# Kernel optimization log

Measured on AMD Instinct MI355X. Metric: run time of the kernel, lower is better.

The kernel has to match this reference:

```python
import jax, jax.numpy as jnp
import numpy as np

BN_EPS = 1e-5

def batchnorm(x, gamma, beta):
    # training-mode BatchNorm1d over the row (node/sample) dimension
    mu = jnp.mean(x, axis=0)
    var = jnp.var(x, axis=0)
    return (x - mu) * jax.lax.rsqrt(var + BN_EPS) * gamma + beta

def gin_mean(h, src, dst, n):
    # DGL GINConv(apply_func=None, aggregator='mean', eps=0):
    # h_new = h + mean_{u in N(v)} h_u
    ones = jnp.ones((src.shape[0],), h.dtype)
    deg = jax.ops.segment_sum(ones, dst, num_segments=n)
    agg = jax.ops.segment_sum(h[src], dst, num_segments=n)
    return h + agg / jnp.maximum(deg, 1.0)[:, None]

def setup_inputs() -> dict:
    key = jax.random.key(0)
    ks = jax.random.split(key, 12)
    N, E, B, K = 10000, 160000, 64, 10
    DIN, D, DH = 20, 512, 256
    x = jax.random.normal(ks[0], (N, DIN), dtype=jnp.float32)
    edge_src = jax.random.randint(ks[1], (E,), 0, N, dtype=jnp.int32)
    edge_dst = jax.random.randint(ks[2], (E,), 0, N, dtype=jnp.int32)
    node2graph = jnp.sort(jax.random.randint(ks[3], (N,), 0, B, dtype=jnp.int32))
    pg_emb = jax.random.normal(ks[4], (B, D), dtype=jnp.float32)
    neigh_emb = jax.random.normal(ks[5], (B, K, D), dtype=jnp.float32)
    s = lambda i, shp: jax.random.normal(ks[i], shp, dtype=jnp.float32) * 0.02
    return dict(
        x=x, pg_emb=pg_emb, neigh_emb=neigh_emb,
        W_init=s(6, (DIN, D)), b_init=jnp.zeros((D,), jnp.float32),
        g1=jnp.ones((D,), jnp.float32), be1=jnp.zeros((D,), jnp.float32),
        g2=jnp.ones((D,), jnp.float32), be2=jnp.zeros((D,), jnp.float32),
        W_fc=s(7, (3 * D, DH)), b_fc=jnp.zeros((DH,), jnp.float32),
        W_fc2=s(8, (DH, DH)), b_fc2=jnp.zeros((DH,), jnp.float32),
        W_fc3=s(9, (DH, DH)), b_fc3=jnp.zeros((DH,), jnp.float32),
        W_fc4=s(10, (DH, 1)), b_fc4=jnp.zeros((1,), jnp.float32),
        gb=jnp.ones((DH,), jnp.float32), bb=jnp.zeros((DH,), jnp.float32),
        gb2=jnp.ones((DH,), jnp.float32), bb2=jnp.zeros((DH,), jnp.float32),
        gb3=jnp.ones((DH,), jnp.float32), bb3=jnp.zeros((DH,), jnp.float32),
        edge_src=edge_src, edge_dst=edge_dst, node2graph=node2graph,
    )

def reference(x, pg_emb, neigh_emb, W_init, b_init, g1, be1, g2, be2,
              W_fc, b_fc, W_fc2, b_fc2, W_fc3, b_fc3, W_fc4, b_fc4,
              gb, bb, gb2, bb2, gb3, bb3, edge_src, edge_dst, node2graph):
    N = x.shape[0]
    B, K, D = neigh_emb.shape
    # two GIN(mean) layers with BN+ReLU on the batched graph
    h = x @ W_init + b_init                                   # [N, 512]
    h = jax.nn.relu(batchnorm(gin_mean(h, edge_src, edge_dst, N), g1, be1))
    h = jax.nn.relu(batchnorm(gin_mean(h, edge_src, edge_dst, N), g2, be2))
    # dgl.mean_nodes: per-graph mean readout
    cnt = jax.ops.segment_sum(jnp.ones((N,), h.dtype), node2graph, num_segments=B)
    qemb = jax.ops.segment_sum(h, node2graph, num_segments=B) / jnp.maximum(cnt, 1.0)[:, None]
    a = jnp.concatenate([qemb, pg_emb], axis=1)               # [B, 2D]
    a = jnp.broadcast_to(a[:, None, :], (B, K, 2 * D))        # repeat per candidate
    b = jnp.concatenate([a, neigh_emb], axis=-1).reshape(B * K, 3 * D)
    H = jax.nn.relu(batchnorm(b @ W_fc + b_fc, gb, bb))
    H2 = jax.nn.relu(batchnorm(H @ W_fc2 + b_fc2, gb2, bb2))
    H3 = jax.nn.relu(batchnorm(H2 @ W_fc3 + b_fc3, gb3, bb3))
    pred = jax.nn.sigmoid(H3 @ W_fc4 + b_fc4)                 # [B*K, 1]
    return pred.reshape(B, K)
```

## Files before the change

### kernel.cpp

```cpp
#include <hip/hip_runtime.h>
#include <hip/hip_bf16.h>
#include <math.h>

#define N_NODES 10000
#define N_EDGES 160000
#define D 512
#define DIN 20
#define B 64
#define KC 10
#define DH 256
#define NROW (B*KC)
#define BN_EPS 1e-5f

#define ZCOUNT 36352
#define Z4 (ZCOUNT/4)
#define D4 (N_NODES/4)
#define IM_ROWS 8
#define IM_UNITS (N_NODES/IM_ROWS)
#define DEG_BLOCKS 625
#define GWAVES 4
#define GBLOCKS 1250
#define F1_NS 6
#define F1_ROWS 8
#define F1_KS 256
#define FM_ROWS 4
#define FM_KS 128
#define FM_NS 2

struct P {
  const float *x, *pg, *neigh, *Winit, *binit;
  const float *g1, *be1, *g2, *be2;
  const float *Wfc, *bfc, *W2, *b2, *W3, *b3, *W4, *b4;
  const float *gbA, *bbA, *gbB, *bbB, *gbC, *bbC;
  const int *esrc, *edst, *n2g;
  unsigned short *hb0, *hb1, *hb2;
  float *zbuf, *csum1, *csq1, *csum2, *csq2;
  float *s1,*q1,*s2,*q2,*s3,*q3, *qemb;
  float *G1,*G2,*G3,*part;
  int *degi,*rowstart,*cursor,*csr,*gstart;
  float *out;
};

__device__ __forceinline__ void f4acc(float4& a, const float4 v){
  a.x += v.x; a.y += v.y; a.z += v.z; a.w += v.w;
}
__device__ __forceinline__ void mk_affine(const float4 s, const float4 q, const float4 g,
                                          const float4 b, float4& sc, float4& sh){
  const float invN = 1.0f/(float)N_NODES;
  float mu, var, rs;
  mu = s.x*invN; var = q.x*invN - mu*mu; rs = rsqrtf(var+BN_EPS); sc.x = rs*g.x; sh.x = b.x - mu*sc.x;
  mu = s.y*invN; var = q.y*invN - mu*mu; rs = rsqrtf(var+BN_EPS); sc.y = rs*g.y; sh.y = b.y - mu*sc.y;
  mu = s.z*invN; var = q.z*invN - mu*mu; rs = rsqrtf(var+BN_EPS); sc.z = rs*g.z; sh.z = b.z - mu*sc.z;
  mu = s.w*invN; var = q.w*invN - mu*mu; rs = rsqrtf(var+BN_EPS); sc.w = rs*g.w; sh.w = b.w - mu*sc.w;
}
__device__ __forceinline__ float4 aff_relu(const float4 v, const float4 sc, const float4 sh){
  float4 o;
  o.x = fmaxf(fmaf(v.x, sc.x, sh.x), 0.0f);
  o.y = fmaxf(fmaf(v.y, sc.y, sh.y), 0.0f);
  o.z = fmaxf(fmaf(v.z, sc.z, sh.z), 0.0f);
  o.w = fmaxf(fmaf(v.w, sc.w, sh.w), 0.0f);
  return o;
}
__device__ __forceinline__ void bf_unpack(const uint4 u, float4& lo, float4& hi){
  lo.x = __uint_as_float(u.x << 16); lo.y = __uint_as_float(u.x & 0xffff0000u);
  lo.z = __uint_as_float(u.y << 16); lo.w = __uint_as_float(u.y & 0xffff0000u);
  hi.x = __uint_as_float(u.z << 16); hi.y = __uint_as_float(u.z & 0xffff0000u);
  hi.z = __uint_as_float(u.w << 16); hi.w = __uint_as_float(u.w & 0xffff0000u);
}
__device__ __forceinline__ unsigned bf_pack2(float a, float b){
  unsigned ua = __float_as_uint(a); ua = (ua + 0x7fffu + ((ua>>16)&1u)) >> 16;
  unsigned ub = __float_as_uint(b); ub = (ub + 0x7fffu + ((ub>>16)&1u)) & 0xffff0000u;
  return (ua & 0xffffu) | ub;
}
__device__ __forceinline__ unsigned short bf_pack1(float a){
  unsigned ua = __float_as_uint(a); return (unsigned short)((ua + 0x7fffu + ((ua>>16)&1u)) >> 16);
}

template<bool FUSED>
__device__ __forceinline__ void gather_body(const P& p,
    const unsigned short* __restrict__ hin, unsigned short* __restrict__ hout,
    const float* pcs, const float* pcq, const float* pgm, const float* pbt,
    float* cs, float* cq, float* red){
  int t = threadIdx.x;
  int lane = t & 63;
  int wave = t >> 6;
  int wid  = blockIdx.x*GWAVES + wave;
  int tot  = gridDim.x*GWAVES;
  const uint4* hb4 = (const uint4*)hin;
  float4 scA, shA, scB, shB;
  if (FUSED){
    mk_affine(((const float4*)pcs)[2*lane],   ((const float4*)pcq)[2*lane],
              ((const float4*)pgm)[2*lane],   ((const float4*)pbt)[2*lane],   scA, shA);
    mk_affine(((const float4*)pcs)[2*lane+1], ((const float4*)pcq)[2*lane+1],
              ((const float4*)pgm)[2*lane+1], ((const float4*)pbt)[2*lane+1], scB, shB);
  }
  float4 sLo = make_float4(0,0,0,0), sHi = make_float4(0,0,0,0);
  float4 qLo = make_float4(0,0,0,0), qHi = make_float4(0,0,0,0);
  for (int node = wid; node < N_NODES; node += tot){
    int start = p.rowstart[node], end = p.rowstart[node+1];
    float4 aLo = make_float4(0,0,0,0), aHi = make_float4(0,0,0,0);
    float4 bLo = make_float4(0,0,0,0), bHi = make_float4(0,0,0,0);
    for (int base = start; base < end; base += 64){
      int cnt = end - base; if (cnt > 64) cnt = 64;
      int myidx = (lane < cnt) ? p.csr[base+lane] : 0;
      int j = 0;
      for (; j+8 <= cnt; j += 8){
        uint4 u[8];
        #pragma unroll
        for (int k = 0; k < 8; ++k){
          int idx = __shfl(myidx, j+k, 64);
          u[k] = hb4[(size_t)idx*64 + lane];
        }
        #pragma unroll
        for (int k = 0; k < 8; ++k){
          float4 lo, hi; bf_unpack(u[k], lo, hi);
          if (FUSED){ lo = aff_relu(lo, scA, shA); hi = aff_relu(hi, scB, shB); }
          if (k & 1){ f4acc(bLo, lo); f4acc(bHi, hi); }
          else      { f4acc(aLo, lo); f4acc(aHi, hi); }
        }
      }
      for (; j < cnt; ++j){
        int idx = __shfl(myidx, j, 64);
        uint4 u0 = hb4[(size_t)idx*64 + lane];
        float4 lo, hi; bf_unpack(u0, lo, hi);
        if (FUSED){ lo = aff_relu(lo, scA, shA); hi = aff_relu(hi, scB, shB); }
        f4acc(aLo, lo); f4acc(aHi, hi);
      }
    }
    float inv = 1.0f/fmaxf((float)(end-start), 1.0f);
    uint4 us = hb4[(size_t)node*64 + lane];
    float4 hLo, hHi; bf_unpack(us, hLo, hHi);
    if (FUSED){ hLo = aff_relu(hLo, scA, shA); hHi = aff_relu(hHi, scB, shB); }
    float4 oLo, oHi;
    oLo.x = hLo.x + (aLo.x+bLo.x)*inv;  oLo.y = hLo.y + (aLo.y+bLo.y)*inv;
    oLo.z = hLo.z + (aLo.z+bLo.z)*inv;  oLo.w = hLo.w + (aLo.w+bLo.w)*inv;
    oHi.x = hHi.x + (aHi.x+bHi.x)*inv;  oHi.y = hHi.y + (aHi.y+bHi.y)*inv;
    oHi.z = hHi.z + (aHi.z+bHi.z)*inv;  oHi.w = hHi.w + (aHi.w+bHi.w)*inv;
    uint4 ou;
    ou.x = bf_pack2(oLo.x, oLo.y); ou.y = bf_pack2(oLo.z, oLo.w);
    ou.z = bf_pack2(oHi.x, oHi.y); ou.w = bf_pack2(oHi.z, oHi.w);
    ((uint4*)hout)[(size_t)node*64 + lane] = ou;
    f4acc(sLo, oLo); f4acc(sHi, oHi);
    qLo.x += oLo.x*oLo.x; qLo.y += oLo.y*oLo.y; qLo.z += oLo.z*oLo.z; qLo.w += oLo.w*oLo.w;
    qHi.x += oHi.x*oHi.x; qHi.y += oHi.y*oHi.y; qHi.z += oHi.z*oHi.z; qHi.w += oHi.w*oHi.w;
  }
  float* my = red + wave*1024;
  int c = 8*lane;
  *((float4*)&my[c])      = sLo;  *((float4*)&my[c+4])     = sHi;
  *((float4*)&my[512+c])  = qLo;  *((float4*)&my[512+c+4]) = qHi;
  __syncthreads();
  for (int e = t; e < 1024; e += 256){
    float v = red[e] + red[1024+e] + red[2048+e] + red[3072+e];
    if (e < 512) atomicAdd(&cs[e], v);
    else         atomicAdd(&cq[e-512], v);
  }
}

__global__ __launch_bounds__(256) void k_setup(P p){
  int b = blockIdx.x, nb = gridDim.x, t = threadIdx.x;
  for (int i4 = b*256 + t; i4 < Z4 + D4; i4 += nb*256){
    if (i4 < Z4) ((float4*)p.zbuf)[i4] = make_float4(0.f,0.f,0.f,0.f);
    else         ((int4*)p.degi)[i4 - Z4] = make_int4(0,0,0,0);
  }
  if (b == 0 && t <= B){
    int lo = 0, hi = N_NODES;
    while (lo < hi){ int mid = (lo+hi)>>1; if (p.n2g[mid] < t) lo = mid+1; else hi = mid; }
    p.gstart[t] = lo;
  }
}

__global__ __launch_bounds__(256) void k_deg_init(P p){
  __shared__ float xs[IM_ROWS*DIN];
  int t = threadIdx.x;
  if (blockIdx.x < DEG_BLOCKS){
    int e = blockIdx.x*256 + t;
    if (e < N_EDGES) atomicAdd(&p.degi[p.edst[e]], 1);
    return;
  }
  int unit = blockIdx.x - DEG_BLOCKS;
  float wlo[DIN], whi[DIN];
  #pragma unroll
  for (int k = 0; k < DIN; ++k){ wlo[k] = p.Winit[k*D + t]; whi[k] = p.Winit[k*D + t + 256]; }
  float b0 = p.binit[t], b1 = p.binit[t+256];
  int r0 = unit*IM_ROWS;
  for (int i = t; i < IM_ROWS*DIN; i += 256) xs[i] = p.x[(size_t)r0*DIN + i];
  __syncthreads();
  for (int rr = 0; rr < IM_ROWS; ++rr){
    float a0 = b0, a1 = b1;
    #pragma unroll
    for (int k = 0; k < DIN; ++k){
      float xv = xs[rr*DIN + k];
      a0 += xv*wlo[k]; a1 += xv*whi[k];
    }
    p.hb0[(size_t)(r0+rr)*D + t]       = bf_pack1(a0);
    p.hb0[(size_t)(r0+rr)*D + t + 256] = bf_pack1(a1);
  }
}

__global__ __launch_bounds__(256) void k_scan(P p){
  __shared__ int part[256];
  int t = threadIdx.x;
  const int PER = (N_NODES + 255)/256;
  int base = t*PER;
  int s = 0;
  for (int i = 0; i < PER; ++i){ int idx = base+i; if (idx < N_NODES) s += p.degi[idx]; }
  part[t] = s;
  __syncthreads();
  for (int off = 1; off < 256; off <<= 1){
    int v = (t >= off) ? part[t-off] : 0;
    __syncthreads();
    part[t] += v;
    __syncthreads();
  }
  int run = (t > 0) ? part[t-1] : 0;
  for (int i = 0; i < PER; ++i){
    int idx = base+i;
    if (idx < N_NODES){ p.rowstart[idx] = run; p.cursor[idx] = run; run += p.degi[idx]; }
  }
  if (t == 255) p.rowstart[N_NODES] = run;
}

__global__ __launch_bounds__(256) void k_fill(P p){
  int e = blockIdx.x*256 + threadIdx.x;
  if (e < N_EDGES){
    int pos = atomicAdd(&p.cursor[p.edst[e]], 1);
    p.csr[pos] = p.esrc[e];
  }
}

__global__ __launch_bounds__(256) void k_g1(P p){
  __shared__ float red[4096];
  gather_body<false>(p, p.hb0, p.hb1, nullptr,nullptr,nullptr,nullptr, p.csum1, p.csq1, red);
}
__global__ __launch_bounds__(256) void k_g2(P p){
  __shared__ float red[4096];
  gather_body<true>(p, p.hb1, p.hb2, p.csum1, p.csq1, p.g1, p.be1, p.csum2, p.csq2, red);
}

__global__ __launch_bounds__(256) void k_readout(P p){
  __shared__ float red[2048];
  int g = blockIdx.x >> 3, chunk = blockIdx.x & 7;
  int t = threadIdx.x;
  int lane = t & 63, wave = t >> 6;
  const uint4* hb4 = (const uint4*)p.hb2;
  float4 scA, shA, scB, shB;
  mk_affine(((const float4*)p.csum2)[2*lane],   ((const float4*)p.csq2)[2*lane],
            ((const float4*)p.g2)[2*lane],      ((const float4*)p.be2)[2*lane],   scA, shA);
  mk_affine(((const float4*)p.csum2)[2*lane+1], ((const float4*)p.csq2)[2*lane+1],
            ((const float4*)p.g2)[2*lane+1],    ((const float4*)p.be2)[2*lane+1], scB, shB);
  int s = p.gstart[g], e = p.gstart[g+1];
  int rows = e - s;
  int per = (rows + 7)/8;
  int r0 = s + chunk*per;
  int r1 = r0 + per; if (r1 > e) r1 = e;
  float4 aLo = make_float4(0,0,0,0), aHi = make_float4(0,0,0,0);
  for (int r = r0 + wave; r < r1; r += 4){
    uint4 u = hb4[(size_t)r*64 + lane];
    float4 lo, hi; bf_unpack(u, lo, hi);
    lo = aff_relu(lo, scA, shA); hi = aff_relu(hi, scB, shB);
    f4acc(aLo, lo); f4acc(aHi, hi);
  }
  int c = 8*lane;
  *((float4*)&red[wave*512 + c])     = aLo;
  *((float4*)&red[wave*512 + c + 4]) = aHi;
  __syncthreads();
  for (int e2 = t; e2 < 512; e2 += 256){
    float v = red[e2] + red[512+e2] + red[1024+e2] + red[1536+e2];
    atomicAdd(&p.qemb[(size_t)g*D + e2], v);
  }
}

__global__ __launch_bounds__(256) void k_fc1(P p){
  __shared__ float brow[F1_ROWS*F1_KS];
  int t = threadIdx.x;
  int rb = blockIdx.x % 80, ks = blockIdx.x / 80;
  int r0 = rb*F1_ROWS, k0 = ks*F1_KS;
  for (int rr = 0; rr < F1_ROWS; ++rr){
    int r = r0+rr;
    int g = r/KC, k = r - g*KC;
    int j = k0 + t;
    float v;
    if (j < D){
      float invc = 1.0f/fmaxf((float)(p.gstart[g+1]-p.gstart[g]), 1.0f);
      v = p.qemb[(size_t)g*D + j]*invc;
    } else if (j < 2*D){
      v = p.pg[(size_t)g*D + (j-D)];
    } else {
      v = p.neigh[((size_t)g*KC + k)*D + (j-2*D)];
    }
    brow[rr*F1_KS + t] = v;
  }
  __syncthreads();
  float acc[F1_ROWS] = {0.f,0.f,0.f,0.f,0.f,0.f,0.f,0.f};
  #pragma unroll 4
  for (int kk = 0; kk < F1_KS; ++kk){
    float w = p.Wfc[(size_t)(k0+kk)*DH + t];
    #pragma unroll
    for (int rr = 0; rr < F1_ROWS; ++rr) acc[rr] += brow[rr*F1_KS + kk]*w;
  }
  for (int rr = 0; rr < F1_ROWS; ++rr)
    p.part[((size_t)ks*NROW + r0+rr)*DH + t] = acc[rr];
}

__global__ __launch_bounds__(256) void k_reduce(P p, const float* bias, float* outG,
                                                float* s, float* q, int nslice){
  int t = threadIdx.x;
  int r0 = blockIdx.x*8;
  float bval = bias[t];
  float ls = 0.f, lq = 0.f;
  for (int rr = 0; rr < 8; ++rr){
    int r = r0+rr;
    float acc = bval;
    for (int sl = 0; sl < nslice; ++sl) acc += p.part[((size_t)sl*NROW + r)*DH + t];
    outG[(size_t)r*DH + t] = acc;
    ls += acc; lq += acc*acc;
  }
  atomicAdd(&s[t], ls); atomicAdd(&q[t], lq);
}

__global__ __launch_bounds__(256) void k_fcmid(P p, const float* in, const float* ps,
    const float* pq, const float* gamma, const float* beta, const float* W){
  __shared__ float row[FM_ROWS*FM_KS];
  int t = threadIdx.x;
  int r0 = blockIdx.x*FM_ROWS;
  int k0 = blockIdx.y*FM_KS;
  const float invM = 1.0f/(float)NROW;
  #pragma unroll
  for (int i = 0; i < 2; ++i){
    int idx = t + i*256;
    int rr = idx >> 7, kk = idx & 127;
    int c = k0 + kk;
    float mu = ps[c]*invM;
    float var = pq[c]*invM - mu*mu;
    float rs = rsqrtf(var + BN_EPS);
    float v = in[(size_t)(r0+rr)*DH + c];
    row[rr*FM_KS + kk] = fmaxf((v-mu)*rs*gamma[c] + beta[c], 0.0f);
  }
  __syncthreads();
  float acc[FM_ROWS] = {0.f,0.f,0.f,0.f};
  #pragma unroll 4
  for (int kk = 0; kk < FM_KS; ++kk){
    float w = W[(size_t)(k0+kk)*DH + t];
    #pragma unroll
    for (int rr = 0; rr < FM_ROWS; ++rr) acc[rr] += row[rr*FM_KS + kk]*w;
  }
  for (int rr = 0; rr < FM_ROWS; ++rr)
    p.part[((size_t)blockIdx.y*NROW + r0+rr)*DH + t] = acc[rr];
}

__global__ __launch_bounds__(256) void k_final(P p){
  int t = threadIdx.x;
  int wave = t>>6, lane = t&63;
  int r = blockIdx.x*4 + wave;
  const float invM = 1.0f/(float)NROW;
  float sum = 0.f;
  #pragma unroll
  for (int j = 0; j < 4; ++j){
    int c = lane + 64*j;
    float mu = p.s3[c]*invM;
    float var = p.q3[c]*invM - mu*mu;
    float rs = rsqrtf(var+BN_EPS);
    float v = p.G3[(size_t)r*DH + c];
    v = fmaxf((v-mu)*rs*p.gbC[c] + p.bbC[c], 0.0f);
    sum += v*p.W4[c];
  }
  #pragma unroll
  for (int off = 32; off > 0; off >>= 1) sum += __shfl_down(sum, off, 64);
  if (lane == 0){
    float z = sum + p.b4[0];
    p.out[r] = 1.0f/(1.0f + expf(-z));
  }
}

extern "C" void kernel_launch(void* const* d_in, const int* in_sizes, int n_in,
                              void* d_out, int out_size, void* d_ws, size_t ws_size,
                              hipStream_t stream) {
  P p;
  p.x     = (const float*)d_in[0];
  p.pg    = (const float*)d_in[1];
  p.neigh = (const float*)d_in[2];
  p.Winit = (const float*)d_in[3];
  p.binit = (const float*)d_in[4];
  p.g1    = (const float*)d_in[5];
  p.be1   = (const float*)d_in[6];
  p.g2    = (const float*)d_in[7];
  p.be2   = (const float*)d_in[8];
  p.Wfc   = (const float*)d_in[9];
  p.bfc   = (const float*)d_in[10];
  p.W2    = (const float*)d_in[11];
  p.b2    = (const float*)d_in[12];
  p.W3    = (const float*)d_in[13];
  p.b3    = (const float*)d_in[14];
  p.W4    = (const float*)d_in[15];
  p.b4    = (const float*)d_in[16];
  p.gbA   = (const float*)d_in[17];
  p.bbA   = (const float*)d_in[18];
  p.gbB   = (const float*)d_in[19];
  p.bbB   = (const float*)d_in[20];
  p.gbC   = (const float*)d_in[21];
  p.bbC   = (const float*)d_in[22];
  p.esrc  = (const int*)d_in[23];
  p.edst  = (const int*)d_in[24];
  p.n2g   = (const int*)d_in[25];
  p.out   = (float*)d_out;

  float* ws = (float*)d_ws;
  size_t off = 0;
  p.hb0 = (unsigned short*)(ws + off); off += (size_t)N_NODES*D/2;
  p.hb1 = (unsigned short*)(ws + off); off += (size_t)N_NODES*D/2;
  p.hb2 = (unsigned short*)(ws + off); off += (size_t)N_NODES*D/2;
  p.zbuf  = ws + off;
  p.csum1 = ws + off; off += 512;
  p.csq1  = ws + off; off += 512;
  p.csum2 = ws + off; off += 512;
  p.csq2  = ws + off; off += 512;
  p.s1    = ws + off; off += 256;
  p.q1    = ws + off; off += 256;
  p.s2    = ws + off; off += 256;
  p.q2    = ws + off; off += 256;
  p.s3    = ws + off; off += 256;
  p.q3    = ws + off; off += 256;
  p.qemb  = ws + off; off += (size_t)B*D;
  p.G1   = ws + off; off += (size_t)NROW*DH;
  p.G2   = ws + off; off += (size_t)NROW*DH;
  p.G3   = ws + off; off += (size_t)NROW*DH;
  p.part = ws + off; off += (size_t)F1_NS*NROW*DH;
  p.degi     = (int*)(ws + off); off += N_NODES;
  p.rowstart = (int*)(ws + off); off += N_NODES + 1;
  p.cursor   = (int*)(ws + off); off += N_NODES;
  p.csr      = (int*)(ws + off); off += N_EDGES;
  p.gstart   = (int*)(ws + off); off += B + 1;

  k_setup<<<64, 256, 0, stream>>>(p);
  k_deg_init<<<DEG_BLOCKS + IM_UNITS, 256, 0, stream>>>(p);
  k_scan<<<1, 256, 0, stream>>>(p);
  k_fill<<<(N_EDGES+255)/256, 256, 0, stream>>>(p);
  k_g1<<<GBLOCKS, 256, 0, stream>>>(p);
  k_g2<<<GBLOCKS, 256, 0, stream>>>(p);
  k_readout<<<512, 256, 0, stream>>>(p);
  k_fc1<<<480, 256, 0, stream>>>(p);
  k_reduce<<<NROW/8, 256, 0, stream>>>(p, p.bfc, p.G1, p.s1, p.q1, F1_NS);
  k_fcmid<<<dim3(NROW/FM_ROWS, FM_NS), 256, 0, stream>>>(p, p.G1, p.s1, p.q1, p.gbA, p.bbA, p.W2);
  k_reduce<<<NROW/8, 256, 0, stream>>>(p, p.b2, p.G2, p.s2, p.q2, FM_NS);
  k_fcmid<<<dim3(NROW/FM_ROWS, FM_NS), 256, 0, stream>>>(p, p.G2, p.s2, p.q2, p.gbB, p.bbB, p.W3);
  k_reduce<<<NROW/8, 256, 0, stream>>>(p, p.b3, p.G3, p.s3, p.q3, FM_NS);
  k_final<<<NROW/4, 256, 0, stream>>>(p);
}
```

Measured before the change: 240.5 us.

## Fuse FC tail into one persistent kernel with software grid barriers

Replaces the six tail kernels (reduce, two fcmid+reduce pairs, final) with a single 160-block kernel that uses atomic-counter grid barriers between layers. Each block computes the full K=256 dot product, so split-K partials and their separate reduction pass go away. It also halves GBLOCKS for the GIN kernels and enlarges the zeroed region so the barrier counter gets cleared. The intent is to remove launch overhead and intermediate traffic. The cost is that correctness depends on all 160 blocks being co-resident, and the spin-wait barrier has its own latency.

New measurement: 213.0 us. 11.4% less time.

```diff
diff --git a/kernel.cpp b/kernel.cpp
--- a/kernel.cpp
+++ b/kernel.cpp
@@ -12,20 +12,18 @@
 #define NROW (B*KC)
 #define BN_EPS 1e-5f
 
-#define ZCOUNT 36352
+#define ZCOUNT 36356
 #define Z4 (ZCOUNT/4)
 #define D4 (N_NODES/4)
 #define IM_ROWS 8
 #define IM_UNITS (N_NODES/IM_ROWS)
 #define DEG_BLOCKS 625
 #define GWAVES 4
-#define GBLOCKS 1250
+#define GBLOCKS 625
 #define F1_NS 6
 #define F1_ROWS 8
 #define F1_KS 256
-#define FM_ROWS 4
-#define FM_KS 128
-#define FM_NS 2
+#define TB 160
 
 struct P {
   const float *x, *pg, *neigh, *Winit, *binit;
@@ -36,6 +34,7 @@
   unsigned short *hb0, *hb1, *hb2;
   float *zbuf, *csum1, *csq1, *csum2, *csq2;
   float *s1,*q1,*s2,*q2,*s3,*q3, *qemb;
+  int *bar;
   float *G1,*G2,*G3,*part;
   int *degi,*rowstart,*cursor,*csr,*gstart;
   float *out;
@@ -302,73 +301,90 @@
     p.part[((size_t)ks*NROW + r0+rr)*DH + t] = acc[rr];
 }
 
-__global__ __launch_bounds__(256) void k_reduce(P p, const float* bias, float* outG,
-                                                float* s, float* q, int nslice){
-  int t = threadIdx.x;
-  int r0 = blockIdx.x*8;
-  float bval = bias[t];
-  float ls = 0.f, lq = 0.f;
-  for (int rr = 0; rr < 8; ++rr){
-    int r = r0+rr;
-    float acc = bval;
-    for (int sl = 0; sl < nslice; ++sl) acc += p.part[((size_t)sl*NROW + r)*DH + t];
-    outG[(size_t)r*DH + t] = acc;
-    ls += acc; lq += acc*acc;
-  }
-  atomicAdd(&s[t], ls); atomicAdd(&q[t], lq);
-}
-
-__global__ __launch_bounds__(256) void k_fcmid(P p, const float* in, const float* ps,
-    const float* pq, const float* gamma, const float* beta, const float* W){
-  __shared__ float row[FM_ROWS*FM_KS];
-  int t = threadIdx.x;
-  int r0 = blockIdx.x*FM_ROWS;
-  int k0 = blockIdx.y*FM_KS;
+__device__ __forceinline__ void grid_bar(int* cnt, int target){
+  __syncthreads();
+  if (threadIdx.x == 0){
+    atomicAdd(cnt, 1);
+    while (atomicAdd(cnt, 0) < target) ;
+  }
+  __syncthreads();
+}
+
+__device__ __forceinline__ void fc_layer(const float* in, const float* ps, const float* pq,
+    const float* gamma, const float* beta, const float* W, const float* bias,
+    float* outG, float* s, float* q, int b, int t, float* row){
+  int r0 = b*4;
   const float invM = 1.0f/(float)NROW;
   #pragma unroll
-  for (int i = 0; i < 2; ++i){
+  for (int i = 0; i < 4; ++i){
     int idx = t + i*256;
-    int rr = idx >> 7, kk = idx & 127;
-    int c = k0 + kk;
-    float mu = ps[c]*invM;
-    float var = pq[c]*invM - mu*mu;
+    int rr = idx >> 8, kk = idx & 255;
+    float mu = ps[kk]*invM;
+    float var = pq[kk]*invM - mu*mu;
     float rs = rsqrtf(var + BN_EPS);
-    float v = in[(size_t)(r0+rr)*DH + c];
-    row[rr*FM_KS + kk] = fmaxf((v-mu)*rs*gamma[c] + beta[c], 0.0f);
-  }
-  __syncthreads();
-  float acc[FM_ROWS] = {0.f,0.f,0.f,0.f};
+    float v = in[(size_t)(r0+rr)*DH + kk];
+    row[rr*DH + kk] = fmaxf((v-mu)*rs*gamma[kk] + beta[kk], 0.0f);
+  }
+  __syncthreads();
+  float bv = bias[t];
+  float a0 = bv, a1 = bv, a2 = bv, a3 = bv;
   #pragma unroll 4
-  for (int kk = 0; kk < FM_KS; ++kk){
-    float w = W[(size_t)(k0+kk)*DH + t];
+  for (int kk = 0; kk < DH; ++kk){
+    float w = W[(size_t)kk*DH + t];
+    a0 += row[0*DH+kk]*w; a1 += row[1*DH+kk]*w;
+    a2 += row[2*DH+kk]*w; a3 += row[3*DH+kk]*w;
+  }
+  outG[(size_t)(r0+0)*DH + t] = a0;
+  outG[(size_t)(r0+1)*DH + t] = a1;
+  outG[(size_t)(r0+2)*DH + t] = a2;
+  outG[(size_t)(r0+3)*DH + t] = a3;
+  atomicAdd(&s[t], a0+a1+a2+a3);
+  atomicAdd(&q[t], a0*a0 + a1*a1 + a2*a2 + a3*a3);
+  __syncthreads();
+}
+
+__global__ __launch_bounds__(256, 2) void k_tail(P p){
+  __shared__ float row[4*DH];
+  int t = threadIdx.x, b = blockIdx.x;
+  {
+    int r0 = b*4;
+    float bval = p.bfc[t];
+    float ls = 0.f, lq = 0.f;
+    for (int rr = 0; rr < 4; ++rr){
+      int r = r0+rr;
+      float acc = bval;
+      for (int sl = 0; sl < F1_NS; ++sl) acc += p.part[((size_t)sl*NROW + r)*DH + t];
+      p.G1[(size_t)r*DH + t] = acc;
+      ls += acc; lq += acc*acc;
+    }
+    atomicAdd(&p.s1[t], ls); atomicAdd(&p.q1[t], lq);
+  }
+  grid_bar(p.bar, TB);
+  fc_layer(p.G1, p.s1, p.q1, p.gbA, p.bbA, p.W2, p.b2, p.G2, p.s2, p.q2, b, t, row);
+  grid_bar(p.bar, 2*TB);
+  fc_layer(p.G2, p.s2, p.q2, p.gbB, p.bbB, p.W3, p.b3, p.G3, p.s3, p.q3, b, t, row);
+  grid_bar(p.bar, 3*TB);
+  {
+    int wave = t>>6, lane = t&63;
+    int r = b*4 + wave;
+    const float invM = 1.0f/(float)NROW;
+    float sum = 0.f;
     #pragma unroll
-    for (int rr = 0; rr < FM_ROWS; ++rr) acc[rr] += row[rr*FM_KS + kk]*w;
-  }
-  for (int rr = 0; rr < FM_ROWS; ++rr)
-    p.part[((size_t)blockIdx.y*NROW + r0+rr)*DH + t] = acc[rr];
-}
-
-__global__ __launch_bounds__(256) void k_final(P p){
-  int t = threadIdx.x;
-  int wave = t>>6, lane = t&63;
-  int r = blockIdx.x*4 + wave;
-  const float invM = 1.0f/(float)NROW;
-  float sum = 0.f;
-  #pragma unroll
-  for (int j = 0; j < 4; ++j){
-    int c = lane + 64*j;
-    float mu = p.s3[c]*invM;
-    float var = p.q3[c]*invM - mu*mu;
-    float rs = rsqrtf(var+BN_EPS);
-    float v = p.G3[(size_t)r*DH + c];
-    v = fmaxf((v-mu)*rs*p.gbC[c] + p.bbC[c], 0.0f);
-    sum += v*p.W4[c];
-  }
-  #pragma unroll
-  for (int off = 32; off > 0; off >>= 1) sum += __shfl_down(sum, off, 64);
-  if (lane == 0){
-    float z = sum + p.b4[0];
-    p.out[r] = 1.0f/(1.0f + expf(-z));
+    for (int j = 0; j < 4; ++j){
+      int c = lane + 64*j;
+      float mu = p.s3[c]*invM;
+      float var = p.q3[c]*invM - mu*mu;
+      float rs = rsqrtf(var+BN_EPS);
+      float v = p.G3[(size_t)r*DH + c];
+      v = fmaxf((v-mu)*rs*p.gbC[c] + p.bbC[c], 0.0f);
+      sum += v*p.W4[c];
+    }
+    #pragma unroll
+    for (int off = 32; off > 0; off >>= 1) sum += __shfl_down(sum, off, 64);
+    if (lane == 0){
+      float z = sum + p.b4[0];
+      p.out[r] = 1.0f/(1.0f + expf(-z));
+    }
   }
 }
 
@@ -421,6 +437,7 @@
   p.s3    = ws + off; off += 256;
   p.q3    = ws + off; off += 256;
   p.qemb  = ws + off; off += (size_t)B*D;
+  p.bar   = (int*)(ws + off); off += 4;
   p.G1   = ws + off; off += (size_t)NROW*DH;
   p.G2   = ws + off; off += (size_t)NROW*DH;
   p.G3   = ws + off; off += (size_t)NROW*DH;
@@ -439,10 +456,5 @@
   k_g2<<<GBLOCKS, 256, 0, stream>>>(p);
   k_readout<<<512, 256, 0, stream>>>(p);
   k_fc1<<<480, 256, 0, stream>>>(p);
-  k_reduce<<<NROW/8, 256, 0, stream>>>(p, p.bfc, p.G1, p.s1, p.q1, F1_NS);
-  k_fcmid<<<dim3(NROW/FM_ROWS, FM_NS), 256, 0, stream>>>(p, p.G1, p.s1, p.q1, p.gbA, p.bbA, p.W2);
-  k_reduce<<<NROW/8, 256, 0, stream>>>(p, p.b2, p.G2, p.s2, p.q2, FM_NS);
-  k_fcmid<<<dim3(NROW/FM_ROWS, FM_NS), 256, 0, stream>>>(p, p.G2, p.s2, p.q2, p.gbB, p.bbB, p.W3);
-  k_reduce<<<NROW/8, 256, 0, stream>>>(p, p.b3, p.G3, p.s3, p.q3, FM_NS);
-  k_final<<<NROW/4, 256, 0, stream>>>(p);
-}
+  k_tail<<<TB, 256, 0, stream>>>(p);
+}
```
